# Performance work log

Measured on AMD Instinct MI355X. Metric: run time of the kernel, lower is better.

Reference implementation:

```python
import jax, jax.numpy as jnp
import numpy as np

PATCH_H, PATCH_W = 14, 14
N = PATCH_H * PATCH_W

def _build_adjacency(H, W):
    A = np.zeros((H * W, H * W), dtype=np.float32)
    for i in range(H):
        for j in range(W):
            idx = i * W + j
            for ni, nj in [(i - 1, j), (i + 1, j), (i, j - 1), (i, j + 1)]:
                if 0 <= ni < H and 0 <= nj < W:
                    A[idx, ni * W + nj] = 1.0
    return jnp.asarray(A)

A_ADJ = _build_adjacency(PATCH_H, PATCH_W)          # [N, N]
I_EYE = jnp.eye(N, dtype=jnp.float32)               # [N, N]

def setup_inputs() -> dict:
    key = jax.random.key(0)
    k1, k2 = jax.random.split(key)
    B, C = 256, 768
    S = jax.random.normal(k1, (B, C, PATCH_H, PATCH_W), dtype=jnp.float32)
    attn = jax.random.uniform(k2, (B, 1, PATCH_H, PATCH_W), dtype=jnp.float32)
    lmbd = jnp.array([2.0], dtype=jnp.float32)
    beta = jnp.array([0.1], dtype=jnp.float32)
    return {"S": S, "attn": attn, "lmbd": lmbd, "beta": beta}

def reference(S, attn, lmbd, beta):
    B, C, H, W = S.shape
    lm = lmbd[0]
    bt = beta[0]
    attn5 = attn * 5.0                                      # [B,1,H,W]
    # L2-normalize over channel dim (torch F.normalize, eps=1e-12)
    S_flat = S.reshape(B, C, N)                             # [B,C,N]
    norm = jnp.sqrt(jnp.sum(S_flat * S_flat, axis=1, keepdims=True))
    S_flat = S_flat / jnp.maximum(norm, 1e-12)
    # patch-patch similarity Gram matrix
    E = jnp.einsum('bcn,bcm->bnm', S_flat, S_flat)          # [B,N,N]
    E = (E + 1.0) * 0.5
    # graph Laplacian weighted by attention-modulated similarity
    deg = jnp.sum(A_ADJ, axis=-1)                           # [N]
    DmA = jnp.diag(deg) - A_ADJ                             # [N,N]
    L = DmA[None, :, :] * (lm * E - 1.0) + 1e-6 * I_EYE[None, :, :]
    # Newton-Schulz iterations for pseudo-inverse
    X = jnp.swapaxes(L, -1, -2) * 0.01
    twoI = 2.0 * I_EYE[None, :, :]
    for _ in range(4):
        X = X @ (twoI - L @ X)
    # diffuse attention through pseudo-inverse
    Fd = jnp.einsum('bnm,bm->bn', X, attn5.reshape(B, N))   # [B,N]
    F_diff = bt * (Fd - jnp.tanh(Fd / (bt + 1e-8)))         # tanh-shrinkage
    F_map = F_diff.reshape(B, 1, H, W)
    S_new = S * (1.0 + F_map)
    return (S_new, F_map)
```

## Files before the change

### kernel.cpp

```cpp
#include <hip/hip_runtime.h>
#include <cstdint>

#define PN 196
#define PC 768
#define KC 16

template<int NCH>
__global__ __launch_bounds__(256) void adb_reduce(
    const float* __restrict__ S, float* __restrict__ partials)
{
    constexpr int CPB = PC / NCH;
    const int b   = blockIdx.y;
    const int ch  = blockIdx.x;
    const int tid = threadIdx.x;

    __shared__ float rows[KC * PN];

    const float* Sb = S + (size_t)b * PC * PN + (size_t)ch * CPB * PN;

    const bool lane = tid < PN;
    const int n = lane ? tid : 0;
    const int i = n / 14, j = n % 14;
    const bool has_r = lane && (j < 13);
    const bool has_d = lane && (i < 13);
    const int ir = n + (has_r ? 1  : 0);
    const int id = n + (has_d ? 14 : 0);

    float acc_s = 0.f, acc_r = 0.f, acc_d = 0.f;

    for (int c0 = 0; c0 < CPB; c0 += KC) {
        __syncthreads();
        const float4* src = (const float4*)(Sb + c0 * PN);
        float4* dst = (float4*)rows;
        #pragma unroll
        for (int k = 0; k < 4; k++) {
            int idx = tid + k * 256;
            if (idx < KC * PN / 4) dst[idx] = src[idx];
        }
        __syncthreads();
        if (lane) {
            #pragma unroll
            for (int cc = 0; cc < KC; cc++) {
                const float* r = rows + cc * PN;
                float s = r[n];
                acc_s += s * s;
                acc_r += s * r[ir];
                acc_d += s * r[id];
            }
        }
    }

    if (lane) {
        float* P = partials + ((size_t)b * NCH + ch) * 3 * PN;
        P[0 * PN + n] = acc_s;
        P[1 * PN + n] = acc_r;
        P[2 * PN + n] = acc_d;
    }
}

template<int NCH>
__global__ __launch_bounds__(256) void adb_solve(
    const float* __restrict__ partials, const float* __restrict__ attn,
    const float* __restrict__ lmbd, const float* __restrict__ beta,
    float* __restrict__ Fmap, float* __restrict__ Gmap)
{
    const int b   = blockIdx.x;
    const int tid = threadIdx.x;

    __shared__ float rnorm[PN];
    __shared__ float srs[PN];
    __shared__ float sds[PN];
    __shared__ float buf[2][PN];

    const bool lane = tid < PN;
    const int n = lane ? tid : 0;
    const int i = n / 14, j = n % 14;
    const bool has_l = lane && (j > 0);
    const bool has_r = lane && (j < 13);
    const bool has_u = lane && (i > 0);
    const bool has_d = lane && (i < 13);
    const int il = n - (has_l ? 1  : 0);
    const int ir = n + (has_r ? 1  : 0);
    const int iu = n - (has_u ? 14 : 0);
    const int id = n + (has_d ? 14 : 0);

    float acc_s = 0.f, acc_r = 0.f, acc_d = 0.f;
    if (lane) {
        const float* P = partials + (size_t)b * NCH * 3 * PN;
        #pragma unroll
        for (int ch = 0; ch < NCH; ch++) {
            const float* Pc = P + ch * 3 * PN;
            acc_s += Pc[0 * PN + n];
            acc_r += Pc[1 * PN + n];
            acc_d += Pc[2 * PN + n];
        }
    }

    const float lm = lmbd[0];
    const float bt = beta[0];

    float rn = 0.f, va = 0.f;
    if (lane) {
        rn = 1.0f / fmaxf(sqrtf(acc_s), 1e-12f);
        rnorm[n] = rn;
        srs[n]   = acc_r;
        sds[n]   = acc_d;
        va = attn[(size_t)b * PN + n] * 5.0f;
    }
    __syncthreads();

    float Lc = 0.f, Ll = 0.f, Lr = 0.f, Lu = 0.f, Ld = 0.f;
    if (lane) {
        float deg = (float)((has_l?1:0) + (has_r?1:0) + (has_u?1:0) + (has_d?1:0));
        float Enn = (acc_s * rn * rn + 1.f) * 0.5f;
        Lc = deg * (lm * Enn - 1.f) + 1e-6f;
        if (has_r) Lr = 1.f - lm * ((acc_r   * rn * rnorm[ir] + 1.f) * 0.5f);
        if (has_l) Ll = 1.f - lm * ((srs[il] * rn * rnorm[il] + 1.f) * 0.5f);
        if (has_d) Ld = 1.f - lm * ((acc_d   * rn * rnorm[id] + 1.f) * 0.5f);
        if (has_u) Lu = 1.f - lm * ((sds[iu] * rn * rnorm[iu] + 1.f) * 0.5f);
    }

    int p = 0;
    auto mv = [&](float src) -> float {
        if (lane) buf[p][n] = src;
        __syncthreads();
        float r = 0.f;
        if (lane) {
            r = Lc * buf[p][n]  + Ll * buf[p][il] + Lr * buf[p][ir]
              + Lu * buf[p][iu] + Ld * buf[p][id];
        }
        p ^= 1;
        return r;
    };

    float vv = 0.01f * mv(va);

    #pragma unroll
    for (int stage = 0; stage < 4; stage++) {
        float w = vv;
        const int k = 1 << stage;
        for (int it = 0; it < k; it++) {
            float t  = mv(w);
            float s2 = mv(t);
            w -= 0.01f * s2;
        }
        vv += w;
    }

    if (lane) {
        float Fd = vv;
        float Fdiff = bt * (Fd - tanhf(Fd / (bt + 1e-8f)));
        Fmap[(size_t)b * PN + n] = Fdiff;
        Gmap[(size_t)b * PN + n] = 1.0f + Fdiff;
    }
}

__global__ __launch_bounds__(256) void adb_scale(
    const float* __restrict__ S, const float* __restrict__ Gmap,
    float* __restrict__ out)
{
    const int b   = blockIdx.y;
    const int tid = threadIdx.x;

    __shared__ float Gs[PN + 3];
    const float* Gb = Gmap + (size_t)b * PN;
    if (tid < PN / 4) ((float4*)Gs)[tid] = ((const float4*)Gb)[tid];
    if (tid >= 64 && tid < 67) Gs[PN + (tid - 64)] = Gb[tid - 64];
    __syncthreads();

    const int off = blockIdx.x * 1024 + tid * 4;
    const int n0  = off % PN;
    const size_t base = (size_t)b * PC * PN + off;
    float4 sv = *(const float4*)(S + base);
    float4 o;
    o.x = sv.x * Gs[n0];
    o.y = sv.y * Gs[n0 + 1];
    o.z = sv.z * Gs[n0 + 2];
    o.w = sv.w * Gs[n0 + 3];
    *(float4*)(out + base) = o;
}

extern "C" void kernel_launch(void* const* d_in, const int* in_sizes, int n_in,
                              void* d_out, int out_size, void* d_ws, size_t ws_size,
                              hipStream_t stream) {
    const float* S    = (const float*)d_in[0];
    const float* attn = (const float*)d_in[1];
    const float* lmbd = (const float*)d_in[2];
    const float* beta = (const float*)d_in[3];

    const int B = in_sizes[1] / PN;

    float* Snew = (float*)d_out;
    float* Fmap = (float*)d_out + (size_t)B * PC * PN;
    float* ws   = (float*)d_ws;

    const size_t need8 = ((size_t)B * 8 * 3 * PN + (size_t)B * PN) * sizeof(float);
    const size_t need2 = ((size_t)B * 2 * 3 * PN + (size_t)B * PN) * sizeof(float);
    const size_t need1 = ((size_t)B * 1 * 3 * PN + (size_t)B * PN) * sizeof(float);

    if (ws_size >= need8) {
        float* partials = ws;
        float* Gmap = ws + (size_t)B * 8 * 3 * PN;
        adb_reduce<8><<<dim3(8, B), 256, 0, stream>>>(S, partials);
        adb_solve<8><<<B, 256, 0, stream>>>(partials, attn, lmbd, beta, Fmap, Gmap);
        adb_scale<<<dim3((PC * PN) / 1024, B), 256, 0, stream>>>(S, Gmap, Snew);
    } else if (ws_size >= need2) {
        float* partials = ws;
        float* Gmap = ws + (size_t)B * 2 * 3 * PN;
        adb_reduce<2><<<dim3(2, B), 256, 0, stream>>>(S, partials);
        adb_solve<2><<<B, 256, 0, stream>>>(partials, attn, lmbd, beta, Fmap, Gmap);
        adb_scale<<<dim3((PC * PN) / 1024, B), 256, 0, stream>>>(S, Gmap, Snew);
    } else {
        float* partials = ws;
        float* Gmap = ws + (size_t)B * 1 * 3 * PN;
        (void)need1;
        adb_reduce<1><<<dim3(1, B), 256, 0, stream>>>(S, partials);
        adb_solve<1><<<B, 256, 0, stream>>>(partials, attn, lmbd, beta, Fmap, Gmap);
        adb_scale<<<dim3((PC * PN) / 1024, B), 256, 0, stream>>>(S, Gmap, Snew);
    }
}
```

Measured before the change: 300.0 us.

## Run Laplacian solve in one wavefront with 2x2 blocks and lane shuffles

The per-batch iterative solve now uses a single 64-lane wavefront in which each lane owns a 2x2 patch block. Neighbour values move through cross-lane shuffles instead of shared memory, removing a block-wide barrier per sparse matvec. The reduce kernel also replaces per-thread boundary index selection with fixed neighbour offsets into a padded shared buffer, relying on later masking of edge coefficients. Occupancy per block is lower, and the unmasked edge reads pick up unrelated data that must be discarded downstream.

```diff
diff --git a/kernel.cpp b/kernel.cpp
--- a/kernel.cpp
+++ b/kernel.cpp
@@ -14,17 +14,12 @@
     const int ch  = blockIdx.x;
     const int tid = threadIdx.x;
 
-    __shared__ float rows[KC * PN];
+    __shared__ __align__(16) float rows[KC * PN + 16];
 
     const float* Sb = S + (size_t)b * PC * PN + (size_t)ch * CPB * PN;
 
     const bool lane = tid < PN;
     const int n = lane ? tid : 0;
-    const int i = n / 14, j = n % 14;
-    const bool has_r = lane && (j < 13);
-    const bool has_d = lane && (i < 13);
-    const int ir = n + (has_r ? 1  : 0);
-    const int id = n + (has_d ? 14 : 0);
 
     float acc_s = 0.f, acc_r = 0.f, acc_d = 0.f;
 
@@ -39,13 +34,14 @@
         }
         __syncthreads();
         if (lane) {
+            const float* r0 = rows + n;
             #pragma unroll
             for (int cc = 0; cc < KC; cc++) {
-                const float* r = rows + cc * PN;
-                float s = r[n];
+                const float* r = r0 + cc * PN;
+                float s = r[0];
                 acc_s += s * s;
-                acc_r += s * r[ir];
-                acc_d += s * r[id];
+                acc_r += s * r[1];
+                acc_d += s * r[14];
             }
         }
     }
@@ -59,99 +55,155 @@
 }
 
 template<int NCH>
-__global__ __launch_bounds__(256) void adb_solve(
+__global__ __launch_bounds__(64) void adb_solve(
     const float* __restrict__ partials, const float* __restrict__ attn,
     const float* __restrict__ lmbd, const float* __restrict__ beta,
     float* __restrict__ Fmap, float* __restrict__ Gmap)
 {
-    const int b   = blockIdx.x;
-    const int tid = threadIdx.x;
-
-    __shared__ float rnorm[PN];
-    __shared__ float srs[PN];
-    __shared__ float sds[PN];
-    __shared__ float buf[2][PN];
-
-    const bool lane = tid < PN;
-    const int n = lane ? tid : 0;
-    const int i = n / 14, j = n % 14;
-    const bool has_l = lane && (j > 0);
-    const bool has_r = lane && (j < 13);
-    const bool has_u = lane && (i > 0);
-    const bool has_d = lane && (i < 13);
-    const int il = n - (has_l ? 1  : 0);
-    const int ir = n + (has_r ? 1  : 0);
-    const int iu = n - (has_u ? 14 : 0);
-    const int id = n + (has_d ? 14 : 0);
-
-    float acc_s = 0.f, acc_r = 0.f, acc_d = 0.f;
-    if (lane) {
+    const int b  = blockIdx.x;
+    const int L  = threadIdx.x;
+    const int i2 = L / 7, j2 = L % 7;
+    const bool act = (L < 49) && (i2 < 7);
+
+    const int n00 = act ? ((2 * i2) * 14 + 2 * j2) : 0;
+    const int nn0 = n00, nn1 = n00 + 1, nn2 = n00 + 14, nn3 = n00 + 15;
+
+    float as0 = 0.f, as1 = 0.f, as2 = 0.f, as3 = 0.f;
+    float ar0 = 0.f, ar1 = 0.f, ar2 = 0.f, ar3 = 0.f;
+    float ad0 = 0.f, ad1 = 0.f, ad2 = 0.f, ad3 = 0.f;
+    if (act) {
         const float* P = partials + (size_t)b * NCH * 3 * PN;
         #pragma unroll
         for (int ch = 0; ch < NCH; ch++) {
             const float* Pc = P + ch * 3 * PN;
-            acc_s += Pc[0 * PN + n];
-            acc_r += Pc[1 * PN + n];
-            acc_d += Pc[2 * PN + n];
+            as0 += Pc[nn0]; as1 += Pc[nn1]; as2 += Pc[nn2]; as3 += Pc[nn3];
+            ar0 += Pc[PN + nn0]; ar1 += Pc[PN + nn1];
+            ar2 += Pc[PN + nn2]; ar3 += Pc[PN + nn3];
+            ad0 += Pc[2 * PN + nn0]; ad1 += Pc[2 * PN + nn1];
+            ad2 += Pc[2 * PN + nn2]; ad3 += Pc[2 * PN + nn3];
         }
     }
 
     const float lm = lmbd[0];
     const float bt = beta[0];
 
-    float rn = 0.f, va = 0.f;
-    if (lane) {
-        rn = 1.0f / fmaxf(sqrtf(acc_s), 1e-12f);
-        rnorm[n] = rn;
-        srs[n]   = acc_r;
-        sds[n]   = acc_d;
-        va = attn[(size_t)b * PN + n] * 5.0f;
-    }
-    __syncthreads();
-
-    float Lc = 0.f, Ll = 0.f, Lr = 0.f, Lu = 0.f, Ld = 0.f;
-    if (lane) {
-        float deg = (float)((has_l?1:0) + (has_r?1:0) + (has_u?1:0) + (has_d?1:0));
-        float Enn = (acc_s * rn * rn + 1.f) * 0.5f;
-        Lc = deg * (lm * Enn - 1.f) + 1e-6f;
-        if (has_r) Lr = 1.f - lm * ((acc_r   * rn * rnorm[ir] + 1.f) * 0.5f);
-        if (has_l) Ll = 1.f - lm * ((srs[il] * rn * rnorm[il] + 1.f) * 0.5f);
-        if (has_d) Ld = 1.f - lm * ((acc_d   * rn * rnorm[id] + 1.f) * 0.5f);
-        if (has_u) Lu = 1.f - lm * ((sds[iu] * rn * rnorm[iu] + 1.f) * 0.5f);
-    }
-
-    int p = 0;
-    auto mv = [&](float src) -> float {
-        if (lane) buf[p][n] = src;
-        __syncthreads();
-        float r = 0.f;
-        if (lane) {
-            r = Lc * buf[p][n]  + Ll * buf[p][il] + Lr * buf[p][ir]
-              + Lu * buf[p][iu] + Ld * buf[p][id];
-        }
-        p ^= 1;
-        return r;
+    float rn0 = 1.0f / fmaxf(sqrtf(as0), 1e-12f);
+    float rn1 = 1.0f / fmaxf(sqrtf(as1), 1e-12f);
+    float rn2 = 1.0f / fmaxf(sqrtf(as2), 1e-12f);
+    float rn3 = 1.0f / fmaxf(sqrtf(as3), 1e-12f);
+
+    const int sl_l = (j2 > 0) ? L - 1 : L;
+    const int sl_r = (j2 < 6) ? L + 1 : L;
+    const int sl_u = (i2 > 0) ? L - 7 : L;
+    const int sl_d = (i2 < 6) ? L + 7 : L;
+
+    float rnL0 = __shfl(rn1, sl_l, 64);
+    float rnL2 = __shfl(rn3, sl_l, 64);
+    float rnR1 = __shfl(rn0, sl_r, 64);
+    float rnR3 = __shfl(rn2, sl_r, 64);
+    float rnU0 = __shfl(rn2, sl_u, 64);
+    float rnU1 = __shfl(rn3, sl_u, 64);
+    float rnD2 = __shfl(rn0, sl_d, 64);
+    float rnD3 = __shfl(rn1, sl_d, 64);
+    float srL0 = __shfl(ar1, sl_l, 64);
+    float srL2 = __shfl(ar3, sl_l, 64);
+    float sdU0 = __shfl(ad2, sl_u, 64);
+    float sdU1 = __shfl(ad3, sl_u, 64);
+
+    const bool hl0 = (j2 > 0), hl2 = (j2 > 0);
+    const bool hr1 = (j2 < 6), hr3 = (j2 < 6);
+    const bool hu0 = (i2 > 0), hu1 = (i2 > 0);
+    const bool hd2 = (i2 < 6), hd3 = (i2 < 6);
+
+    const float deg0 = (hl0 ? 1.f : 0.f) + 1.f + (hu0 ? 1.f : 0.f) + 1.f;
+    const float deg1 = 1.f + (hr1 ? 1.f : 0.f) + (hu1 ? 1.f : 0.f) + 1.f;
+    const float deg2 = (hl2 ? 1.f : 0.f) + 1.f + 1.f + (hd2 ? 1.f : 0.f);
+    const float deg3 = 1.f + (hr3 ? 1.f : 0.f) + 1.f + (hd3 ? 1.f : 0.f);
+
+    auto cdiag = [&](float as, float rn, float deg) {
+        float Enn = (as * rn * rn + 1.f) * 0.5f;
+        return deg * (lm * Enn - 1.f) + 1e-6f;
     };
-
-    float vv = 0.01f * mv(va);
+    auto coff = [&](float dot, float rna, float rnb) {
+        return 1.f - lm * ((dot * rna * rnb + 1.f) * 0.5f);
+    };
+
+    const float Lc0 = cdiag(as0, rn0, deg0);
+    const float Lc1 = cdiag(as1, rn1, deg1);
+    const float Lc2 = cdiag(as2, rn2, deg2);
+    const float Lc3 = cdiag(as3, rn3, deg3);
+
+    const float Ll0 = hl0 ? coff(srL0, rn0, rnL0) : 0.f;
+    const float Ll1 =       coff(ar0,  rn1, rn0);
+    const float Ll2 = hl2 ? coff(srL2, rn2, rnL2) : 0.f;
+    const float Ll3 =       coff(ar2,  rn3, rn2);
+
+    const float Lr0 =       coff(ar0,  rn0, rn1);
+    const float Lr1 = hr1 ? coff(ar1,  rn1, rnR1) : 0.f;
+    const float Lr2 =       coff(ar2,  rn2, rn3);
+    const float Lr3 = hr3 ? coff(ar3,  rn3, rnR3) : 0.f;
+
+    const float Lu0 = hu0 ? coff(sdU0, rn0, rnU0) : 0.f;
+    const float Lu1 = hu1 ? coff(sdU1, rn1, rnU1) : 0.f;
+    const float Lu2 =       coff(ad0,  rn2, rn0);
+    const float Lu3 =       coff(ad1,  rn3, rn1);
+
+    const float Ld0 =       coff(ad0,  rn0, rn2);
+    const float Ld1 =       coff(ad1,  rn1, rn3);
+    const float Ld2 = hd2 ? coff(ad2,  rn2, rnD2) : 0.f;
+    const float Ld3 = hd3 ? coff(ad3,  rn3, rnD3) : 0.f;
+
+    auto mv = [&](float& y0, float& y1, float& y2, float& y3,
+                  float x0, float x1, float x2, float x3) {
+        float xl0 = __shfl(x1, sl_l, 64);
+        float xl2 = __shfl(x3, sl_l, 64);
+        float xr1 = __shfl(x0, sl_r, 64);
+        float xr3 = __shfl(x2, sl_r, 64);
+        float xu0 = __shfl(x2, sl_u, 64);
+        float xu1 = __shfl(x3, sl_u, 64);
+        float xd2 = __shfl(x0, sl_d, 64);
+        float xd3 = __shfl(x1, sl_d, 64);
+        y0 = Lc0 * x0 + Ll0 * xl0 + Lr0 * x1  + Lu0 * xu0 + Ld0 * x2;
+        y1 = Lc1 * x1 + Ll1 * x0  + Lr1 * xr1 + Lu1 * xu1 + Ld1 * x3;
+        y2 = Lc2 * x2 + Ll2 * xl2 + Lr2 * x3  + Lu2 * x0  + Ld2 * xd2;
+        y3 = Lc3 * x3 + Ll3 * x2  + Lr3 * xr3 + Lu3 * x1  + Ld3 * xd3;
+    };
+
+    float a0 = 0.f, a1 = 0.f, a2 = 0.f, a3 = 0.f;
+    if (act) {
+        const float* Ab = attn + (size_t)b * PN;
+        a0 = Ab[nn0] * 5.0f; a1 = Ab[nn1] * 5.0f;
+        a2 = Ab[nn2] * 5.0f; a3 = Ab[nn3] * 5.0f;
+    }
+
+    float v0, v1, v2, v3;
+    mv(v0, v1, v2, v3, a0, a1, a2, a3);
+    v0 *= 0.01f; v1 *= 0.01f; v2 *= 0.01f; v3 *= 0.01f;
 
     #pragma unroll
     for (int stage = 0; stage < 4; stage++) {
-        float w = vv;
+        float w0 = v0, w1 = v1, w2 = v2, w3 = v3;
         const int k = 1 << stage;
         for (int it = 0; it < k; it++) {
-            float t  = mv(w);
-            float s2 = mv(t);
-            w -= 0.01f * s2;
-        }
-        vv += w;
-    }
-
-    if (lane) {
-        float Fd = vv;
-        float Fdiff = bt * (Fd - tanhf(Fd / (bt + 1e-8f)));
-        Fmap[(size_t)b * PN + n] = Fdiff;
-        Gmap[(size_t)b * PN + n] = 1.0f + Fdiff;
+            float t0, t1, t2, t3, s0, s1, s2, s3;
+            mv(t0, t1, t2, t3, w0, w1, w2, w3);
+            mv(s0, s1, s2, s3, t0, t1, t2, t3);
+            w0 -= 0.01f * s0; w1 -= 0.01f * s1;
+            w2 -= 0.01f * s2; w3 -= 0.01f * s3;
+        }
+        v0 += w0; v1 += w1; v2 += w2; v3 += w3;
+    }
+
+    if (act) {
+        auto shrink = [&](float Fd) {
+            return bt * (Fd - tanhf(Fd / (bt + 1e-8f)));
+        };
+        float f0 = shrink(v0), f1 = shrink(v1), f2 = shrink(v2), f3 = shrink(v3);
+        float* Fb = Fmap + (size_t)b * PN;
+        float* Gb = Gmap + (size_t)b * PN;
+        Fb[nn0] = f0; Fb[nn1] = f1; Fb[nn2] = f2; Fb[nn3] = f3;
+        Gb[nn0] = 1.0f + f0; Gb[nn1] = 1.0f + f1;
+        Gb[nn2] = 1.0f + f2; Gb[nn3] = 1.0f + f3;
     }
 }
 
@@ -202,20 +254,20 @@
         float* partials = ws;
         float* Gmap = ws + (size_t)B * 8 * 3 * PN;
         adb_reduce<8><<<dim3(8, B), 256, 0, stream>>>(S, partials);
-        adb_solve<8><<<B, 256, 0, stream>>>(partials, attn, lmbd, beta, Fmap, Gmap);
+        adb_solve<8><<<B, 64, 0, stream>>>(partials, attn, lmbd, beta, Fmap, Gmap);
         adb_scale<<<dim3((PC * PN) / 1024, B), 256, 0, stream>>>(S, Gmap, Snew);
     } else if (ws_size >= need2) {
         float* partials = ws;
         float* Gmap = ws + (size_t)B * 2 * 3 * PN;
         adb_reduce<2><<<dim3(2, B), 256, 0, stream>>>(S, partials);
-        adb_solve<2><<<B, 256, 0, stream>>>(partials, attn, lmbd, beta, Fmap, Gmap);
+        adb_solve<2><<<B, 64, 0, stream>>>(partials, attn, lmbd, beta, Fmap, Gmap);
         adb_scale<<<dim3((PC * PN) / 1024, B), 256, 0, stream>>>(S, Gmap, Snew);
     } else {
         float* partials = ws;
         float* Gmap = ws + (size_t)B * 1 * 3 * PN;
         (void)need1;
         adb_reduce<1><<<dim3(1, B), 256, 0, stream>>>(S, partials);
-        adb_solve<1><<<B, 256, 0, stream>>>(partials, attn, lmbd, beta, Fmap, Gmap);
+        adb_solve<1><<<B, 64, 0, stream>>>(partials, attn, lmbd, beta, Fmap, Gmap);
         adb_scale<<<dim3((PC * PN) / 1024, B), 256, 0, stream>>>(S, Gmap, Snew);
     }
 }
```

After: 299.7 us. No clear change (-0.1%).
